# Optimization experiments

Hardware: AMD Instinct MI355X
Metric: run time of the kernel (lower is better)

## Reference

```python
import jax, jax.numpy as jnp
import numpy as np

EPS = 1e-6
H = 16

def setup_inputs() -> dict:
    key = jax.random.key(0)
    ks = jax.random.split(key, 11)
    B, L, D = 4, 4096, 1024
    sc = 1.0 / np.sqrt(D)
    return {
        "queries": jax.random.normal(ks[0], (B, L, D), jnp.float32),
        "keys": jax.random.normal(ks[1], (B, L, D), jnp.float32),
        "values": jax.random.normal(ks[2], (B, L, D), jnp.float32),
        "Wq": jax.random.normal(ks[3], (D, D), jnp.float32) * sc,
        "bq": jax.random.normal(ks[4], (D,), jnp.float32) * 0.01,
        "Wk": jax.random.normal(ks[5], (D, D), jnp.float32) * sc,
        "bk": jax.random.normal(ks[6], (D,), jnp.float32) * 0.01,
        "Wv": jax.random.normal(ks[7], (D, D), jnp.float32) * sc,
        "bv": jax.random.normal(ks[8], (D,), jnp.float32) * 0.01,
        "Wo": jax.random.normal(ks[9], (D, D), jnp.float32) * sc,
        "bo": jax.random.normal(ks[10], (D,), jnp.float32) * 0.01,
    }

def reference(queries, keys, values, Wq, bq, Wk, bk, Wv, bv, Wo, bo):
    B, L, _ = queries.shape
    S = keys.shape[1]
    # projections + split heads: [B, H, L, dh]
    q = (queries @ Wq + bq).reshape(B, L, H, -1).transpose(0, 2, 1, 3)
    k = (keys @ Wk + bk).reshape(B, S, H, -1).transpose(0, 2, 1, 3)
    v = (values @ Wv + bv).reshape(B, S, H, -1).transpose(0, 2, 1, 3)
    # kernel feature map
    q = jax.nn.sigmoid(q)
    k = jax.nn.sigmoid(k)
    # flow normalization (sink/source)
    sink_incoming = 1.0 / jnp.einsum('nhld,nhd->nhl', q + EPS, k.sum(axis=2) + EPS)
    source_outgoing = 1.0 / jnp.einsum('nhld,nhd->nhl', k + EPS, q.sum(axis=2) + EPS)
    conserved_sink = jnp.einsum('nhld,nhd->nhl', q + EPS,
                                (k * source_outgoing[..., None]).sum(axis=2) + EPS)
    conserved_source = jnp.einsum('nhld,nhd->nhl', k + EPS,
                                  (q * sink_incoming[..., None]).sum(axis=2) + EPS)
    conserved_source = jnp.clip(conserved_source, -1.0, 1.0)
    sink_allocation = jax.nn.sigmoid(conserved_sink * (float(L) / float(S)))
    source_competition = jax.nn.softmax(conserved_source, axis=-1) * float(S)
    # linear attention: kv then q(kv)
    qn = q * sink_incoming[..., None]
    vn = v * source_competition[..., None]
    kv = jnp.einsum('nhld,nhlm->nhdm', k, vn)
    x = jnp.einsum('nhld,nhdm->nhlm', qn, kv) * sink_allocation[..., None]
    x = x.transpose(0, 2, 1, 3).reshape(B, L, -1)
    return x @ Wo + bo
```

## Files before the change

kernel.cpp:

```cpp
#include <hip/hip_runtime.h>

#define Bc 4
#define Lc 4096
#define Dc 1024
#define LDQ 3072
#define Mc (Bc*Lc)
#define EPSc 1e-6f

typedef __bf16 bf16x8 __attribute__((ext_vector_type(8)));
typedef __bf16 bf16x4 __attribute__((ext_vector_type(4)));
typedef float f32x4 __attribute__((ext_vector_type(4)));

typedef __attribute__((address_space(3))) void lds_vt;
typedef const __attribute__((address_space(1))) void gbl_vt;

__device__ __forceinline__ void gll16(const void* g, void* l) {
  __builtin_amdgcn_global_load_lds((gbl_vt*)g, (lds_vt*)l, 16, 0, 0);
}

__global__ __launch_bounds__(256) void conv3(const float* __restrict__ Q, const float* __restrict__ K,
                                             const float* __restrict__ V, __bf16* __restrict__ Y) {
  const float* src = (blockIdx.y == 0) ? Q : (blockIdx.y == 1) ? K : V;
  __bf16* dst = Y + (size_t)blockIdx.y * ((size_t)Mc * Dc);
  const int i = blockIdx.x * 256 + threadIdx.x;
  const float4 v = ((const float4*)src)[i];
  bf16x4 o;
  o[0] = (__bf16)v.x; o[1] = (__bf16)v.y; o[2] = (__bf16)v.z; o[3] = (__bf16)v.w;
  ((bf16x4*)dst)[i] = o;
}

__global__ __launch_bounds__(256) void wt_conv4(const float* __restrict__ W0, const float* __restrict__ W1,
                                                const float* __restrict__ W2, const float* __restrict__ W3,
                                                __bf16* __restrict__ T) {
  const float* W = (blockIdx.z == 0) ? W0 : (blockIdx.z == 1) ? W1 : (blockIdx.z == 2) ? W2 : W3;
  __bf16* Wt = T + (size_t)blockIdx.z * ((size_t)Dc * Dc);
  __shared__ float t[32][33];
  const int n0 = blockIdx.x << 5, k0 = blockIdx.y << 5;
  const int tx = threadIdx.x, ty = threadIdx.y;
#pragma unroll
  for (int i = 0; i < 4; ++i)
    t[ty + 8 * i][tx] = W[(size_t)(k0 + ty + 8 * i) * Dc + n0 + tx];
  __syncthreads();
#pragma unroll
  for (int i = 0; i < 4; ++i)
    Wt[(size_t)(n0 + ty + 8 * i) * Dc + k0 + tx] = (__bf16)t[tx][ty + 8 * i];
}

template <int FUSED>
__global__ __launch_bounds__(256, 4) void gemm128b(
    const __bf16* __restrict__ Aq_, const __bf16* __restrict__ Ak_, const __bf16* __restrict__ Av_,
    const __bf16* __restrict__ Wq_, const __bf16* __restrict__ Wk_, const __bf16* __restrict__ Wv_,
    const float* __restrict__ bq_, const float* __restrict__ bk_, const float* __restrict__ bv_,
    void* __restrict__ Cp, float* __restrict__ qsum, float* __restrict__ ksum) {
  __shared__ __bf16 As[2][128 * 32];
  __shared__ __bf16 Bs[2][128 * 32];
  const int tid = threadIdx.x;
  const int lane = tid & 63, w4 = tid >> 6;
  const int wr = w4 >> 1, wc = w4 & 1;
  const int lf = lane & 15, kq = lane >> 4;

  constexpr int NCT = FUSED ? 24 : 8;
  constexpr int CPX = (128 * NCT) >> 3;
  const int hwlin = blockIdx.x + (blockIdx.y << 7);
  const int swz = (hwlin & 7) * CPX + (hwlin >> 3);
  const int bx = swz / NCT, ct = swz - bx * NCT;
  const int row0 = bx << 7, col0 = ct << 7;
  const int region = FUSED ? (ct >> 3) : 0;
  const int colL = FUSED ? (col0 & 1023) : col0;

  const __bf16* Agl = FUSED ? (region == 0 ? Aq_ : (region == 1 ? Ak_ : Av_)) : Aq_;
  const __bf16* Bgl = FUSED ? (region == 0 ? Wq_ : (region == 1 ? Wk_ : Wv_)) : Wq_;
  const float* biasp = FUSED ? (region == 0 ? bq_ : (region == 1 ? bk_ : bv_)) : bq_;
  const __bf16* Ab_g = Agl + (size_t)row0 * 1024;
  const __bf16* Bb_g = Bgl + (size_t)colL * 1024;

  const int srow = (w4 << 5) + (lane >> 2);
  const int sgd = lane & 3;
  const int ssrc = (sgd ^ ((lane >> 3) & 3)) << 3;
  const size_t aoff0 = (size_t)srow * 1024 + ssrc;
  const size_t aoff1 = (size_t)(srow + 16) * 1024 + ssrc;
  const int ldst0 = srow * 32 + (sgd << 3);
  const int ldst1 = (srow + 16) * 32 + (sgd << 3);

  const int kgsw = (kq ^ ((lf >> 1) & 3)) << 3;
  const int arb = (wr * 64 + lf) * 32 + kgsw;
  const int brb = (wc * 64 + lf) * 32 + kgsw;

  f32x4 acc[4][4] = {};

  for (int t = 0; t < 16; ++t) {
    const int kb = t << 6;
    gll16(Ab_g + aoff0 + kb, &As[0][ldst0]);
    gll16(Ab_g + aoff1 + kb, &As[0][ldst1]);
    gll16(Bb_g + aoff0 + kb, &Bs[0][ldst0]);
    gll16(Bb_g + aoff1 + kb, &Bs[0][ldst1]);
    gll16(Ab_g + aoff0 + kb + 32, &As[1][ldst0]);
    gll16(Ab_g + aoff1 + kb + 32, &As[1][ldst1]);
    gll16(Bb_g + aoff0 + kb + 32, &Bs[1][ldst0]);
    gll16(Bb_g + aoff1 + kb + 32, &Bs[1][ldst1]);
    __syncthreads();
#pragma unroll
    for (int hf = 0; hf < 2; ++hf) {
      bf16x8 af[4], bfr[4];
#pragma unroll
      for (int m = 0; m < 4; ++m) af[m] = *(const bf16x8*)(&As[hf][0] + arb + m * 512);
#pragma unroll
      for (int n = 0; n < 4; ++n) bfr[n] = *(const bf16x8*)(&Bs[hf][0] + brb + n * 512);
#pragma unroll
      for (int m = 0; m < 4; ++m)
#pragma unroll
        for (int n = 0; n < 4; ++n)
          acc[m][n] = __builtin_amdgcn_mfma_f32_16x16x32_bf16(bfr[n], af[m], acc[m][n], 0, 0, 0);
    }
    __syncthreads();
  }

  const int b_of = row0 >> 12;
  const int orow = row0 + wr * 64 + lf;
  const int ocl = wc * 64 + (kq << 2);
#pragma unroll
  for (int n = 0; n < 4; ++n) {
    const int cl = ocl + (n << 4);
    const int cb = colL + cl;
    const f32x4 bb = *(const f32x4*)&biasp[cb];
    f32x4 sacc = {0.f, 0.f, 0.f, 0.f};
#pragma unroll
    for (int m = 0; m < 4; ++m) {
      f32x4 v = acc[m][n] + bb;
      if (FUSED && region < 2) {
#pragma unroll
        for (int r = 0; r < 4; ++r) v[r] = 1.0f / (1.0f + expf(-v[r]));
      }
      if (FUSED) {
        bf16x4 o;
#pragma unroll
        for (int r = 0; r < 4; ++r) o[r] = (__bf16)v[r];
        *(bf16x4*)&((__bf16*)Cp)[(size_t)(orow + (m << 4)) * LDQ + col0 + cl] = o;
      } else {
        *(f32x4*)&((float*)Cp)[(size_t)(orow + (m << 4)) * 1024 + col0 + cl] = v;
      }
      sacc += v;
    }
    if (FUSED && region < 2) {
#pragma unroll
      for (int o = 1; o < 16; o <<= 1) {
        sacc[0] += __shfl_xor(sacc[0], o); sacc[1] += __shfl_xor(sacc[1], o);
        sacc[2] += __shfl_xor(sacc[2], o); sacc[3] += __shfl_xor(sacc[3], o);
      }
      if (lf == 0) {
        float* sums = (region == 0) ? qsum : ksum;
#pragma unroll
        for (int r = 0; r < 4; ++r) atomicAdd(&sums[b_of * 1024 + cb + r], sacc[r]);
      }
    }
  }
}

template <int FUSED>
__global__ __launch_bounds__(256, 2) void gemm256x128(
    const __bf16* __restrict__ Aq_, const __bf16* __restrict__ Ak_, const __bf16* __restrict__ Av_,
    const __bf16* __restrict__ Wq_, const __bf16* __restrict__ Wk_, const __bf16* __restrict__ Wv_,
    const float* __restrict__ bq_, const float* __restrict__ bk_, const float* __restrict__ bv_,
    void* __restrict__ Cp, float* __restrict__ qsum, float* __restrict__ ksum) {
  __shared__ __bf16 As[256 * 32];
  __shared__ __bf16 Bs[128 * 32];
  const int tid = threadIdx.x;
  const int lane = tid & 63, w4 = tid >> 6;
  const int wr = w4 >> 1, wc = w4 & 1;
  const int lf = lane & 15, kq = lane >> 4;

  constexpr int NCT = FUSED ? 24 : 8;
  constexpr int CPX = (64 * NCT) >> 3;
  const int hwlin = blockIdx.x + blockIdx.y * 64;
  const int swz = (hwlin & 7) * CPX + (hwlin >> 3);
  const int bx = swz / NCT, ct = swz - bx * NCT;
  const int row0 = bx << 8, col0 = ct << 7;
  const int region = FUSED ? (ct >> 3) : 0;
  const int colL = FUSED ? (col0 & 1023) : col0;

  const __bf16* Agl = FUSED ? (region == 0 ? Aq_ : (region == 1 ? Ak_ : Av_)) : Aq_;
  const __bf16* Bgl = FUSED ? (region == 0 ? Wq_ : (region == 1 ? Wk_ : Wv_)) : Wq_;
  const float* biasp = FUSED ? (region == 0 ? bq_ : (region == 1 ? bk_ : bv_)) : bq_;
  const __bf16* Ab_g = Agl + (size_t)row0 * 1024;
  const __bf16* Bb_g = Bgl + (size_t)colL * 1024;

  int arow[4], asrc[4];
#pragma unroll
  for (int i = 0; i < 4; ++i) {
    const int g = i * 256 + tid;
    arow[i] = g >> 2;
    asrc[i] = ((g & 3) ^ ((arow[i] >> 1) & 3)) << 3;
  }
  const int kgsw = (kq ^ ((lf >> 1) & 3)) << 3;
  const int arb = (wr * 128 + lf) * 32 + kgsw;
  const int brb = (wc * 64 + lf) * 32 + kgsw;

  f32x4 acc[8][4] = {};

  for (int t = 0; t < 32; ++t) {
    const int kb = t << 5;
#pragma unroll
    for (int i = 0; i < 4; ++i)
      gll16(Ab_g + (size_t)arow[i] * 1024 + kb + asrc[i], &As[(i * 256 + tid) * 8]);
#pragma unroll
    for (int i = 0; i < 2; ++i)
      gll16(Bb_g + (size_t)arow[i] * 1024 + kb + asrc[i], &Bs[(i * 256 + tid) * 8]);
    __syncthreads();
    bf16x8 af[8], bfr[4];
#pragma unroll
    for (int m = 0; m < 8; ++m) af[m] = *(const bf16x8*)(As + arb + m * 512);
#pragma unroll
    for (int n = 0; n < 4; ++n) bfr[n] = *(const bf16x8*)(Bs + brb + n * 512);
#pragma unroll
    for (int m = 0; m < 8; ++m)
#pragma unroll
      for (int n = 0; n < 4; ++n)
        acc[m][n] = __builtin_amdgcn_mfma_f32_16x16x32_bf16(bfr[n], af[m], acc[m][n], 0, 0, 0);
    __syncthreads();
  }

  const int b_of = row0 >> 12;
  const int orow = row0 + wr * 128 + lf;
  const int ocl = wc * 64 + (kq << 2);
#pragma unroll
  for (int n = 0; n < 4; ++n) {
    const int cl = ocl + (n << 4);
    const int cb = colL + cl;
    const f32x4 bb = *(const f32x4*)&biasp[cb];
    f32x4 sacc = {0.f, 0.f, 0.f, 0.f};
#pragma unroll
    for (int m = 0; m < 8; ++m) {
      f32x4 v = acc[m][n] + bb;
      if (FUSED && region < 2) {
#pragma unroll
        for (int r = 0; r < 4; ++r) v[r] = 1.0f / (1.0f + expf(-v[r]));
      }
      if (FUSED) {
        bf16x4 o;
#pragma unroll
        for (int r = 0; r < 4; ++r) o[r] = (__bf16)v[r];
        *(bf16x4*)&((__bf16*)Cp)[(size_t)(orow + (m << 4)) * LDQ + col0 + cl] = o;
      } else {
        *(f32x4*)&((float*)Cp)[(size_t)(orow + (m << 4)) * 1024 + col0 + cl] = v;
      }
      sacc += v;
    }
    if (FUSED && region < 2) {
#pragma unroll
      for (int o = 1; o < 16; o <<= 1) {
        sacc[0] += __shfl_xor(sacc[0], o); sacc[1] += __shfl_xor(sacc[1], o);
        sacc[2] += __shfl_xor(sacc[2], o); sacc[3] += __shfl_xor(sacc[3], o);
      }
      if (lf == 0) {
        float* sums = (region == 0) ? qsum : ksum;
#pragma unroll
        for (int r = 0; r < 4; ++r) atomicAdd(&sums[b_of * 1024 + cb + r], sacc[r]);
      }
    }
  }
}

__global__ __launch_bounds__(256) void r2_flow(const __bf16* __restrict__ Qp, const __bf16* __restrict__ Kp,
                                               const float* __restrict__ ksum, const float* __restrict__ qsum,
                                               float* __restrict__ si,
                                               float* __restrict__ qsi, float* __restrict__ kso) {
  const int blk = blockIdx.x;
  const int chunk = blk & 15, bh = blk >> 4;
  const int b = bh >> 4, h = bh & 15;
  const int d = threadIdx.x & 63, w = threadIdx.x >> 6;
  __shared__ float ksE[64], qsE[64];
  if (threadIdx.x < 64) ksE[threadIdx.x] = ksum[bh * 64 + threadIdx.x] + EPSc;
  else if (threadIdx.x < 128) qsE[threadIdx.x - 64] = qsum[bh * 64 + threadIdx.x - 64] + EPSc;
  __syncthreads();
  const float kE = ksE[d], qE = qsE[d];
  const size_t base = ((size_t)b * Lc) * LDQ + h * 64 + d;
  const size_t obase = (size_t)bh * Lc;
  float qsia = 0.f, ksoa = 0.f;
  const int l0 = chunk * 256;
  for (int i = w; i < 256; i += 4) {
    const int l = l0 + i;
    const size_t idx = base + (size_t)l * LDQ;
    const float qv = (float)Qp[idx], kvv = (float)Kp[idx];
    float a = (qv + EPSc) * kE;
    float c2 = (kvv + EPSc) * qE;
#pragma unroll
    for (int o = 32; o; o >>= 1) { a += __shfl_xor(a, o); c2 += __shfl_xor(c2, o); }
    const float sil = 1.0f / a, sol = 1.0f / c2;
    if (d == 0) si[obase + l] = sil;
    qsia += qv * sil;
    ksoa += kvv * sol;
  }
  atomicAdd(&qsi[bh * 64 + d], qsia);
  atomicAdd(&kso[bh * 64 + d], ksoa);
}

__global__ __launch_bounds__(256) void k5_kv(const __bf16* __restrict__ Kp, const __bf16* __restrict__ Vp,
                                             const float* __restrict__ qsi, float* __restrict__ den,
                                             float* __restrict__ kvout) {
  const int bh = blockIdx.x, chunk = blockIdx.y;
  const int b = bh >> 4, h = bh & 15;
  const int tid = threadIdx.x;
  const int dq = (tid >> 4) << 2;
  const int mq = (tid & 15) << 2;
  __shared__ float qsE[64];
  __shared__ float klds[4][64], vlds[4][64];
  if (tid < 64) qsE[tid] = qsi[bh * 64 + tid] + EPSc;
  __syncthreads();
  float acc[4][4] = {};
  float eacc = 0.f;
  const int r = tid >> 6, c = tid & 63;
  const float qE = qsE[c];
  const size_t rowbase = ((size_t)b * Lc + chunk * 512) * LDQ + h * 64;
  for (int i = 0; i < 512; i += 4) {
    const size_t idx = rowbase + (size_t)(i + r) * LDQ + c;
    const float kvf = (float)Kp[idx];
    const float vvf = (float)Vp[idx];
    float c2 = (kvf + EPSc) * qE;
#pragma unroll
    for (int o = 32; o; o >>= 1) c2 += __shfl_xor(c2, o);
    const float e = expf(fminf(1.0f, fmaxf(-1.0f, c2)));
    if (c == 0) eacc += e;
    __syncthreads();
    klds[r][c] = kvf;
    vlds[r][c] = vvf * e;
    __syncthreads();
#pragma unroll
    for (int rr = 0; rr < 4; ++rr) {
      float kr[4], vr[4];
#pragma unroll
      for (int j = 0; j < 4; ++j) { kr[j] = klds[rr][dq + j]; vr[j] = vlds[rr][mq + j]; }
#pragma unroll
      for (int a = 0; a < 4; ++a)
#pragma unroll
        for (int e2 = 0; e2 < 4; ++e2) acc[a][e2] += kr[a] * vr[e2];
    }
    __syncthreads();
  }
  if (c == 0) atomicAdd(&den[bh], eacc);
#pragma unroll
  for (int a = 0; a < 4; ++a)
#pragma unroll
    for (int e2 = 0; e2 < 4; ++e2)
      atomicAdd(&kvout[(size_t)bh * 4096 + (dq + a) * 64 + mq + e2], acc[a][e2]);
}

__global__ __launch_bounds__(256) void k6_x(const __bf16* __restrict__ Qp,
                                            const float* __restrict__ kvin, const float* __restrict__ si,
                                            const float* __restrict__ kso, const float* __restrict__ den,
                                            __bf16* __restrict__ Xb) {
  const int bh = blockIdx.x, chunk = blockIdx.y;
  const int b = bh >> 4, h = bh & 15;
  const int tid = threadIdx.x, lane = tid & 63, w = tid >> 6;
  const int lf = lane & 15, kq = lane >> 4;
  const float sden = 4096.0f / den[bh];
  f32x4 kE0a = *(const f32x4*)&kso[bh * 64 + kq * 8];
  f32x4 kE0b = *(const f32x4*)&kso[bh * 64 + kq * 8 + 4];
  f32x4 kE1a = *(const f32x4*)&kso[bh * 64 + 32 + kq * 8];
  f32x4 kE1b = *(const f32x4*)&kso[bh * 64 + 32 + kq * 8 + 4];
#pragma unroll
  for (int j = 0; j < 4; ++j) { kE0a[j] += EPSc; kE0b[j] += EPSc; kE1a[j] += EPSc; kE1b[j] += EPSc; }
  __shared__ float ktl[64][66];
  for (int e = tid; e < 4096; e += 256)
    ktl[e & 63][e >> 6] = kvin[(size_t)bh * 4096 + e];
  __syncthreads();
  bf16x8 kh[4][2], kl[4][2];
#pragma unroll
  for (int mi = 0; mi < 4; ++mi)
#pragma unroll
    for (int hf = 0; hf < 2; ++hf) {
      const float* p = &ktl[mi * 16 + lf][hf * 32 + kq * 8];
      bf16x8 hi, lo;
#pragma unroll
      for (int j = 0; j < 8; ++j) {
        const float f = p[j];
        hi[j] = (__bf16)f;
        lo[j] = (__bf16)(f - (float)hi[j]);
      }
      kh[mi][hf] = hi; kl[mi][hf] = lo;
    }
  const size_t bL = (size_t)b * Lc;
  const size_t obase = (size_t)bh * Lc;
#pragma unroll
  for (int gi = 0; gi < 4; ++gi) {
    const int lrow = chunk * 256 + (w * 4 + gi) * 16 + lf;
    const size_t qb = (bL + lrow) * LDQ + h * 64;
    const bf16x8 qf0 = *(const bf16x8*)(Qp + qb + kq * 8);
    const bf16x8 qf1 = *(const bf16x8*)(Qp + qb + 32 + kq * 8);
    float a = 0.f;
#pragma unroll
    for (int j = 0; j < 4; ++j) {
      a += ((float)qf0[j] + EPSc) * kE0a[j];
      a += ((float)qf0[4 + j] + EPSc) * kE0b[j];
      a += ((float)qf1[j] + EPSc) * kE1a[j];
      a += ((float)qf1[4 + j] + EPSc) * kE1b[j];
    }
    a += __shfl_xor(a, 16);
    a += __shfl_xor(a, 32);
    const float sav = 1.0f / (1.0f + expf(-a));
    const float sc = si[obase + lrow] * sav * sden;
    f32x4 acc[4] = {};
#pragma unroll
    for (int mi = 0; mi < 4; ++mi) {
      acc[mi] = __builtin_amdgcn_mfma_f32_16x16x32_bf16(kh[mi][0], qf0, acc[mi], 0, 0, 0);
      acc[mi] = __builtin_amdgcn_mfma_f32_16x16x32_bf16(kh[mi][1], qf1, acc[mi], 0, 0, 0);
      acc[mi] = __builtin_amdgcn_mfma_f32_16x16x32_bf16(kl[mi][0], qf0, acc[mi], 0, 0, 0);
      acc[mi] = __builtin_amdgcn_mfma_f32_16x16x32_bf16(kl[mi][1], qf1, acc[mi], 0, 0, 0);
    }
#pragma unroll
    for (int mi = 0; mi < 4; ++mi) {
      bf16x4 o;
#pragma unroll
      for (int r = 0; r < 4; ++r) o[r] = (__bf16)(acc[mi][r] * sc);
      *(bf16x4*)&Xb[(bL + lrow) * Dc + h * 64 + mi * 16 + (kq << 2)] = o;
    }
  }
}

extern "C" void kernel_launch(void* const* d_in, const int* in_sizes, int n_in,
                              void* d_out, int out_size, void* d_ws, size_t ws_size,
                              hipStream_t stream) {
  const float* Qin = (const float*)d_in[0];
  const float* Kin = (const float*)d_in[1];
  const float* Vin = (const float*)d_in[2];
  const float* Wq = (const float*)d_in[3];
  const float* bq = (const float*)d_in[4];
  const float* Wk = (const float*)d_in[5];
  const float* bk = (const float*)d_in[6];
  const float* Wv = (const float*)d_in[7];
  const float* bv = (const float*)d_in[8];
  const float* Wo = (const float*)d_in[9];
  const float* bo = (const float*)d_in[10];

  const size_t MD = (size_t)Mc * Dc;
  __bf16* Aq = (__bf16*)d_ws;
  __bf16* Ak = Aq + MD;
  __bf16* Av = Ak + MD;
  __bf16* Wqt = Av + MD;
  __bf16* Wkt = Wqt + (size_t)Dc * Dc;
  __bf16* Wvt = Wkt + (size_t)Dc * Dc;
  __bf16* Wot = Wvt + (size_t)Dc * Dc;
  __bf16* QKV = Wot + (size_t)Dc * Dc;
  float* F = (float*)(QKV + (size_t)Mc * LDQ);
  float* ksum = F;
  float* qsum = ksum + 4096;
  float* kso = qsum + 4096;
  float* qsi = kso + 4096;
  float* den = qsi + 4096;
  float* kv = den + 64;
  float* si = kv + 262144;
  __bf16* Xb = Aq;

  hipMemsetAsync(F, 0, (size_t)(4 * 4096 + 64 + 262144) * sizeof(float), stream);

  conv3<<<dim3((int)(MD / 4 / 256), 3), 256, 0, stream>>>(Qin, Kin, Vin, Aq);
  wt_conv4<<<dim3(32, 32, 4), dim3(32, 8), 0, stream>>>(Wq, Wk, Wv, Wo, Wqt);

  gemm128b<1><<<dim3(128, 24), 256, 0, stream>>>(Aq, Ak, Av, Wqt, Wkt, Wvt,
                                                 bq, bk, bv, QKV, qsum, ksum);

  const __bf16* Qp = QKV;
  const __bf16* Kp = QKV + 1024;
  const __bf16* Vp = QKV + 2048;
  r2_flow<<<1024, 256, 0, stream>>>(Qp, Kp, ksum, qsum, si, qsi, kso);
  k5_kv<<<dim3(64, 8), 256, 0, stream>>>(Kp, Vp, qsi, den, kv);
  k6_x<<<dim3(64, 16), 256, 0, stream>>>(Qp, kv, si, kso, den, Xb);

  gemm256x128<0><<<dim3(64, 8), 256, 0, stream>>>(Xb, nullptr, nullptr, Wot, nullptr, nullptr,
                                                  bo, nullptr, nullptr, d_out, nullptr, nullptr);
}
```

Measured before the change: 461.0 us.

## Pipeline QKV GEMM global-to-LDS loads and batch rows in kv accumulation

The fused QKV GEMM main loop now prefetches the next 32-wide K slice into the alternate LDS buffer while MFMAs run on the current one. The old loop loaded both halves and then waited at a barrier before any compute. The k5_kv kernel now stages 16 rows per iteration instead of 4, with one fewer barrier per step, so there is more FMA work per synchronization. The cost is twice as many GEMM loop iterations, each with its own barrier, and more LDS and registers in k5_kv.

```diff
diff --git a/kernel.cpp b/kernel.cpp
--- a/kernel.cpp
+++ b/kernel.cpp
@@ -47,7 +47,7 @@
 }
 
 template <int FUSED>
-__global__ __launch_bounds__(256, 4) void gemm128b(
+__global__ __launch_bounds__(256, 4) void gemm128p(
     const __bf16* __restrict__ Aq_, const __bf16* __restrict__ Ak_, const __bf16* __restrict__ Av_,
     const __bf16* __restrict__ Wq_, const __bf16* __restrict__ Wk_, const __bf16* __restrict__ Wv_,
     const float* __restrict__ bq_, const float* __restrict__ bk_, const float* __restrict__ bv_,
@@ -86,34 +86,35 @@
   const int arb = (wr * 64 + lf) * 32 + kgsw;
   const int brb = (wc * 64 + lf) * 32 + kgsw;
 
+#define STGP(T, U) do { \
+    const int kb_ = (T) << 5; \
+    gll16(Ab_g + aoff0 + kb_, &As[U][ldst0]); \
+    gll16(Ab_g + aoff1 + kb_, &As[U][ldst1]); \
+    gll16(Bb_g + aoff0 + kb_, &Bs[U][ldst0]); \
+    gll16(Bb_g + aoff1 + kb_, &Bs[U][ldst1]); \
+  } while (0)
+
   f32x4 acc[4][4] = {};
 
-  for (int t = 0; t < 16; ++t) {
-    const int kb = t << 6;
-    gll16(Ab_g + aoff0 + kb, &As[0][ldst0]);
-    gll16(Ab_g + aoff1 + kb, &As[0][ldst1]);
-    gll16(Bb_g + aoff0 + kb, &Bs[0][ldst0]);
-    gll16(Bb_g + aoff1 + kb, &Bs[0][ldst1]);
-    gll16(Ab_g + aoff0 + kb + 32, &As[1][ldst0]);
-    gll16(Ab_g + aoff1 + kb + 32, &As[1][ldst1]);
-    gll16(Bb_g + aoff0 + kb + 32, &Bs[1][ldst0]);
-    gll16(Bb_g + aoff1 + kb + 32, &Bs[1][ldst1]);
+  STGP(0, 0);
+  __syncthreads();
+
+  for (int t = 0; t < 32; ++t) {
+    const int u = t & 1;
+    if (t < 31) STGP(t + 1, u ^ 1);
+    bf16x8 af[4], bfr[4];
+#pragma unroll
+    for (int m = 0; m < 4; ++m) af[m] = *(const bf16x8*)(&As[u][0] + arb + m * 512);
+#pragma unroll
+    for (int n = 0; n < 4; ++n) bfr[n] = *(const bf16x8*)(&Bs[u][0] + brb + n * 512);
+#pragma unroll
+    for (int m = 0; m < 4; ++m)
+#pragma unroll
+      for (int n = 0; n < 4; ++n)
+        acc[m][n] = __builtin_amdgcn_mfma_f32_16x16x32_bf16(bfr[n], af[m], acc[m][n], 0, 0, 0);
     __syncthreads();
-#pragma unroll
-    for (int hf = 0; hf < 2; ++hf) {
-      bf16x8 af[4], bfr[4];
-#pragma unroll
-      for (int m = 0; m < 4; ++m) af[m] = *(const bf16x8*)(&As[hf][0] + arb + m * 512);
-#pragma unroll
-      for (int n = 0; n < 4; ++n) bfr[n] = *(const bf16x8*)(&Bs[hf][0] + brb + n * 512);
-#pragma unroll
-      for (int m = 0; m < 4; ++m)
-#pragma unroll
-        for (int n = 0; n < 4; ++n)
-          acc[m][n] = __builtin_amdgcn_mfma_f32_16x16x32_bf16(bfr[n], af[m], acc[m][n], 0, 0, 0);
-    }
-    __syncthreads();
-  }
+  }
+#undef STGP
 
   const int b_of = row0 >> 12;
   const int orow = row0 + wr * 64 + lf;
@@ -303,29 +304,38 @@
   const int dq = (tid >> 4) << 2;
   const int mq = (tid & 15) << 2;
   __shared__ float qsE[64];
-  __shared__ float klds[4][64], vlds[4][64];
+  __shared__ float klds[16][64], vlds[16][64];
   if (tid < 64) qsE[tid] = qsi[bh * 64 + tid] + EPSc;
   __syncthreads();
   float acc[4][4] = {};
   float eacc = 0.f;
-  const int r = tid >> 6, c = tid & 63;
+  const int w = tid >> 6, c = tid & 63;
   const float qE = qsE[c];
   const size_t rowbase = ((size_t)b * Lc + chunk * 512) * LDQ + h * 64;
-  for (int i = 0; i < 512; i += 4) {
-    const size_t idx = rowbase + (size_t)(i + r) * LDQ + c;
-    const float kvf = (float)Kp[idx];
-    const float vvf = (float)Vp[idx];
-    float c2 = (kvf + EPSc) * qE;
-#pragma unroll
-    for (int o = 32; o; o >>= 1) c2 += __shfl_xor(c2, o);
-    const float e = expf(fminf(1.0f, fmaxf(-1.0f, c2)));
-    if (c == 0) eacc += e;
+  for (int i = 0; i < 32; ++i) {
+    float kvf[4], vpe[4];
+#pragma unroll
+    for (int rr = 0; rr < 4; ++rr) {
+      const int lrow = i * 16 + rr * 4 + w;
+      const size_t idx = rowbase + (size_t)lrow * LDQ + c;
+      kvf[rr] = (float)Kp[idx];
+      const float vvf = (float)Vp[idx];
+      float c2 = (kvf[rr] + EPSc) * qE;
+#pragma unroll
+      for (int o = 32; o; o >>= 1) c2 += __shfl_xor(c2, o);
+      const float e = expf(fminf(1.0f, fmaxf(-1.0f, c2)));
+      if (c == 0) eacc += e;
+      vpe[rr] = vvf * e;
+    }
     __syncthreads();
-    klds[r][c] = kvf;
-    vlds[r][c] = vvf * e;
+#pragma unroll
+    for (int rr = 0; rr < 4; ++rr) {
+      klds[rr * 4 + w][c] = kvf[rr];
+      vlds[rr * 4 + w][c] = vpe[rr];
+    }
     __syncthreads();
 #pragma unroll
-    for (int rr = 0; rr < 4; ++rr) {
+    for (int rr = 0; rr < 16; ++rr) {
       float kr[4], vr[4];
 #pragma unroll
       for (int j = 0; j < 4; ++j) { kr[j] = klds[rr][dq + j]; vr[j] = vlds[rr][mq + j]; }
@@ -334,7 +344,6 @@
 #pragma unroll
         for (int e2 = 0; e2 < 4; ++e2) acc[a][e2] += kr[a] * vr[e2];
     }
-    __syncthreads();
   }
   if (c == 0) atomicAdd(&den[bh], eacc);
 #pragma unroll
@@ -455,7 +464,7 @@
   conv3<<<dim3((int)(MD / 4 / 256), 3), 256, 0, stream>>>(Qin, Kin, Vin, Aq);
   wt_conv4<<<dim3(32, 32, 4), dim3(32, 8), 0, stream>>>(Wq, Wk, Wv, Wo, Wqt);
 
-  gemm128b<1><<<dim3(128, 24), 256, 0, stream>>>(Aq, Ak, Av, Wqt, Wkt, Wvt,
+  gemm128p<1><<<dim3(128, 24), 256, 0, stream>>>(Aq, Ak, Av, Wqt, Wkt, Wvt,
                                                  bq, bk, bv, QKV, qsum, ksum);
 
   const __bf16* Qp = QKV;
```

Result: faster. 409.8 us, median of 4 (-11.1%).
